# Optimization experiments

Hardware: AMD Instinct MI355X
Metric: run time of the kernel (lower is better)

## Reference

```python
import jax, jax.numpy as jnp
import numpy as np

B, NUM_OBJ, R, D, C = 1024, 128, 32, 512, 7  # scans, obj slots, rel samples, feat dim, rel classes
N = NUM_OBJ + R  # 160 graph nodes per scan


def setup_inputs() -> dict:
    key = jax.random.key(0)
    ks = jax.random.split(key, 8)
    obj_feats = jax.random.normal(ks[0], (B, NUM_OBJ, D), jnp.float32)
    pairs = jax.random.randint(ks[1], (B, R, 2), 0, NUM_OBJ, dtype=jnp.int32)
    init = lambda k, shape, fan_in: jax.random.normal(k, shape, jnp.float32) / np.float32(np.sqrt(fan_in))
    return {
        "obj_feats": obj_feats,
        "pairs": pairs,
        "fuse_w": init(ks[2], (2 * D, D), 2 * D), "fuse_b": jnp.zeros((D,), jnp.float32),
        "gcn_w": init(ks[3], (D, D), D), "gcn_b": jnp.zeros((D,), jnp.float32),
        "fc1_w": init(ks[4], (D, 256), D), "fc1_b": jnp.zeros((256,), jnp.float32),
        "fc2_w": init(ks[5], (256, 128), 256), "fc2_b": jnp.zeros((128,), jnp.float32),
        "fc3_w": init(ks[6], (128, C), 128), "fc3_b": jnp.zeros((C,), jnp.float32),
    }


def reference(obj_feats, pairs, fuse_w, fuse_b, gcn_w, gcn_b,
              fc1_w, fc1_b, fc2_w, fc2_b, fc3_w, fc3_b):
    # --- init_rel_node (pos_fuse=False): fuse sub/obj features per sampled pair ---
    sub = jnp.take_along_axis(obj_feats, pairs[:, :, 0:1], axis=1)  # [B,R,D]
    obj = jnp.take_along_axis(obj_feats, pairs[:, :, 1:2], axis=1)  # [B,R,D]
    init_rel = jnp.concatenate([sub, obj], axis=-1) @ fuse_w + fuse_b  # [B,R,D]

    # --- X: object node feats in rows [0,NUM_OBJ), rel node feats in rows [NUM_OBJ,N) ---
    X = jnp.concatenate([obj_feats, init_rel], axis=1)  # [B,N,D]

    # --- A: get_graph_gcn_with_rel -- scatter 4 directed edges per pair ---
    b_idx = jnp.arange(B)[:, None]                      # [B,1]
    ridx = NUM_OBJ + jnp.arange(R)[None, :]             # [1,R] rel node index j+num_obj
    p0, p1 = pairs[:, :, 0], pairs[:, :, 1]             # [B,R]
    A = jnp.zeros((B, N, N), jnp.float32)
    A = A.at[b_idx, p0, ridx].set(1.0)
    A = A.at[b_idx, ridx, p1].set(1.0)
    A = A.at[b_idx, p1, ridx].set(1.0)
    A = A.at[b_idx, ridx, p0].set(1.0)

    # --- simpleGCN: relu((A @ X) W + b) ---
    H = jax.nn.relu(jnp.einsum('bnm,bmd->bnd', A, X) @ gcn_w + gcn_b)  # [B,N,D]

    # --- residual: GCN rel-node output + init rel feats ---
    rel_feat = H[:, NUM_OBJ:, :] + init_rel  # [B,R,D]

    # --- proxi_detector (dropout = identity, eval behavior) ---
    h = jax.nn.relu(rel_feat @ fc1_w + fc1_b)
    h = jax.nn.relu(h @ fc2_w + fc2_b)
    logits = h @ fc3_w + fc3_b  # [B,R,C]
    return jax.nn.softmax(logits, axis=-1)
```

## Files before the change

kernel.cpp:

```cpp
#include <hip/hip_runtime.h>
#include <hip/hip_bf16.h>

#define B_    1024
#define NOBJ  128
#define RREL  32
#define DIM   512
#define MTOT  32768

typedef __bf16 bf16x8 __attribute__((ext_vector_type(8)));
typedef float  f32x4  __attribute__((ext_vector_type(4)));
typedef unsigned short us;

__device__ __forceinline__ us f2bf(float f) {
    unsigned int u = __float_as_uint(f);
    u += 0x7FFFu + ((u >> 16) & 1u);
    return (us)(u >> 16);
}
__device__ __forceinline__ float bf2f(us h) {
    return __uint_as_float(((unsigned int)h) << 16);
}

__device__ __forceinline__ void load16_to_lds(const us* g, us* l) {
    __builtin_amdgcn_global_load_lds((const __attribute__((address_space(1))) void*)g,
                                     (__attribute__((address_space(3))) void*)l,
                                     16, 0, 0);
}

__global__ __launch_bounds__(256) void gather_kernel(
        const float* __restrict__ obj, const int* __restrict__ pairs,
        us* __restrict__ As, us* __restrict__ Msum) {
    int t = threadIdx.x;
    int g = t >> 7;
    int c = t & 127;
    int base = blockIdx.x * 8;
#pragma unroll
    for (int rr = 0; rr < 4; ++rr) {
        int m  = base + rr * 2 + g;
        int b  = m >> 5;
        int p0 = pairs[(m << 1) + 0];
        int p1 = pairs[(m << 1) + 1];
        const float4* srow = (const float4*)(obj + (size_t)(b * NOBJ + p0) * DIM);
        const float4* orow = (const float4*)(obj + (size_t)(b * NOBJ + p1) * DIM);
        float4 s4 = srow[c];
        float4 o4 = orow[c];
        size_t arow = (size_t)m * 1024;
        ushort4 sb = make_ushort4(f2bf(s4.x), f2bf(s4.y), f2bf(s4.z), f2bf(s4.w));
        ushort4 ob = make_ushort4(f2bf(o4.x), f2bf(o4.y), f2bf(o4.z), f2bf(o4.w));
        *(ushort4*)(As + arow + c * 4)       = sb;
        *(ushort4*)(As + arow + 512 + c * 4) = ob;
        float4 mz = s4;
        if (p0 != p1) { mz.x += o4.x; mz.y += o4.y; mz.z += o4.z; mz.w += o4.w; }
        *(ushort4*)(Msum + (size_t)m * 512 + c * 4) =
            make_ushort4(f2bf(mz.x), f2bf(mz.y), f2bf(mz.z), f2bf(mz.w));
    }
}

__global__ __launch_bounds__(256) void prep_weights(
        const float* __restrict__ fw, const float* __restrict__ gw,
        const float* __restrict__ w1, const float* __restrict__ w2,
        us* __restrict__ WfT, us* __restrict__ WgT,
        us* __restrict__ W1T, us* __restrict__ W2T) {
    __shared__ float t32[32][33];
    int id = blockIdx.x;
    const float* in; us* out; int K, N, local;
    if (id < 512)      { in = fw; out = WfT; K = 1024; N = 512; local = id; }
    else if (id < 768) { in = gw; out = WgT; K = 512;  N = 512; local = id - 512; }
    else if (id < 896) { in = w1; out = W1T; K = 512;  N = 256; local = id - 768; }
    else               { in = w2; out = W2T; K = 256;  N = 128; local = id - 896; }
    int tilesN = N >> 5;
    int bk = (local / tilesN) * 32;
    int bn = (local % tilesN) * 32;
    int t  = threadIdx.x;
    int tx = t & 31, ty = t >> 5;
#pragma unroll
    for (int i = 0; i < 4; ++i)
        t32[ty + i * 8][tx] = in[(size_t)(bk + ty + i * 8) * N + bn + tx];
    __syncthreads();
#pragma unroll
    for (int i = 0; i < 4; ++i)
        out[(size_t)(bn + ty + i * 8) * K + bk + tx] = f2bf(t32[tx][ty + i * 8]);
}

__global__ __launch_bounds__(256, 2) void gemm_fused12(
        const us* __restrict__ As,
        const us* __restrict__ Msum,
        const us* __restrict__ WfT,
        const us* __restrict__ WgT,
        const float* __restrict__ fuse_b, const float* __restrict__ gcn_b,
        us* __restrict__ rf) {
    __shared__ __align__(16) us ldsA[128 * 32];
    __shared__ __align__(16) us ldsB[128 * 32];

    int tid  = threadIdx.x;
    int wid  = tid >> 6;
    int lane = tid & 63;
    int wm   = wid & 1;
    int wn   = wid >> 1;
    int m0   = blockIdx.x * 128;
    int n0   = blockIdx.y * 128;

    f32x4 accF[4][4], accG[4][4];
#pragma unroll
    for (int i = 0; i < 4; ++i)
#pragma unroll
        for (int j = 0; j < 4; ++j)
#pragma unroll
            for (int k = 0; k < 4; ++k) { accF[i][j][k] = 0.0f; accG[i][j][k] = 0.0f; }

    int r = tid >> 2, c = tid & 3;
    us* la0 = ldsA + wid * 512;
    us* la1 = ldsA + 2048 + wid * 512;
    us* lb0 = ldsB + wid * 512;
    us* lb1 = ldsB + 2048 + wid * 512;

    int arow = wm * 64 + (lane & 15);
    int brow = wn * 64 + (lane & 15);
    int koff = (lane >> 4) * 8;

    {
        const us* ag0 = As + (size_t)(m0 + r)      * 1024 + c * 8;
        const us* ag1 = As + (size_t)(m0 + 64 + r) * 1024 + c * 8;
        const us* bg0 = WfT + (size_t)(n0 + r)      * 1024 + c * 8;
        const us* bg1 = WfT + (size_t)(n0 + 64 + r) * 1024 + c * 8;
        for (int k0 = 0; k0 < 1024; k0 += 32) {
            __syncthreads();
            load16_to_lds(ag0 + k0, la0);
            load16_to_lds(ag1 + k0, la1);
            load16_to_lds(bg0 + k0, lb0);
            load16_to_lds(bg1 + k0, lb1);
            __syncthreads();
            bf16x8 a[4], b[4];
#pragma unroll
            for (int i = 0; i < 4; ++i)
                a[i] = *(const bf16x8*)(ldsA + (arow + i * 16) * 32 + koff);
#pragma unroll
            for (int j = 0; j < 4; ++j)
                b[j] = *(const bf16x8*)(ldsB + (brow + j * 16) * 32 + koff);
#pragma unroll
            for (int i = 0; i < 4; ++i)
#pragma unroll
                for (int j = 0; j < 4; ++j)
                    accF[i][j] = __builtin_amdgcn_mfma_f32_16x16x32_bf16(a[i], b[j], accF[i][j], 0, 0, 0);
        }
    }
    {
        const us* ag0 = Msum + (size_t)(m0 + r)      * 512 + c * 8;
        const us* ag1 = Msum + (size_t)(m0 + 64 + r) * 512 + c * 8;
        const us* bg0 = WgT + (size_t)(n0 + r)      * 512 + c * 8;
        const us* bg1 = WgT + (size_t)(n0 + 64 + r) * 512 + c * 8;
        for (int k0 = 0; k0 < 512; k0 += 32) {
            __syncthreads();
            load16_to_lds(ag0 + k0, la0);
            load16_to_lds(ag1 + k0, la1);
            load16_to_lds(bg0 + k0, lb0);
            load16_to_lds(bg1 + k0, lb1);
            __syncthreads();
            bf16x8 a[4], b[4];
#pragma unroll
            for (int i = 0; i < 4; ++i)
                a[i] = *(const bf16x8*)(ldsA + (arow + i * 16) * 32 + koff);
#pragma unroll
            for (int j = 0; j < 4; ++j)
                b[j] = *(const bf16x8*)(ldsB + (brow + j * 16) * 32 + koff);
#pragma unroll
            for (int i = 0; i < 4; ++i)
#pragma unroll
                for (int j = 0; j < 4; ++j)
                    accG[i][j] = __builtin_amdgcn_mfma_f32_16x16x32_bf16(a[i], b[j], accG[i][j], 0, 0, 0);
        }
    }

    int crow  = wm * 64 + (lane >> 4) * 4;
    int ccol0 = wn * 64 + (lane & 15);
    float bf_[4], bg_[4];
#pragma unroll
    for (int j = 0; j < 4; ++j) {
        bf_[j] = fuse_b[n0 + ccol0 + j * 16];
        bg_[j] = gcn_b [n0 + ccol0 + j * 16];
    }
#pragma unroll
    for (int i = 0; i < 4; ++i)
#pragma unroll
        for (int j = 0; j < 4; ++j) {
            int col = n0 + ccol0 + j * 16;
#pragma unroll
            for (int jj = 0; jj < 4; ++jj) {
                int row = m0 + crow + i * 16 + jj;
                float v = fmaxf(accG[i][j][jj] + bg_[j], 0.0f) + accF[i][j][jj] + bf_[j];
                rf[(size_t)row * 512 + col] = f2bf(v);
            }
        }
}

#define H1S 264
#define H2S 136
__global__ __launch_bounds__(256, 2) void tail_kernel(
        const us* __restrict__ rf,
        const us* __restrict__ W1T,
        const us* __restrict__ W2T,
        const float* __restrict__ b1, const float* __restrict__ b2,
        const float* __restrict__ w3, const float* __restrict__ b3,
        float* __restrict__ out) {
    __shared__ __align__(16) unsigned char pool[57888];
    us*    sA   = (us*)(pool);
    us*    sB   = (us*)(pool + 4096);
    us*    sH2  = (us*)(pool);
    us*    sH1  = (us*)(pool + 20480);
    float* sRed = (float*)(pool + 20480);
    float* sW3  = (float*)(pool + 54272);
    float* sB3  = (float*)(pool + 57856);

    int tid  = threadIdx.x;
    int wid  = tid >> 6;
    int lane = tid & 63;
    int m0   = blockIdx.x * 64;

    for (int i = tid; i < 128 * 7; i += 256) sW3[i] = w3[i];
    if (tid < 7) sB3[tid] = b3[tid];

    int r = tid >> 2, c = tid & 3;
    int koff = (lane >> 4) * 8;
    int l15  = lane & 15;

    f32x4 acc1[4][4];
#pragma unroll
    for (int i = 0; i < 4; ++i)
#pragma unroll
        for (int j = 0; j < 4; ++j)
#pragma unroll
            for (int k = 0; k < 4; ++k) acc1[i][j][k] = 0.0f;

    {
        const us* ag = rf + (size_t)(m0 + r) * 512 + c * 8;
        us* la = sA + wid * 512;
        for (int k0 = 0; k0 < 512; k0 += 32) {
            __syncthreads();
            load16_to_lds(ag + k0, la);
#pragma unroll
            for (int q = 0; q < 4; ++q)
                load16_to_lds(W1T + (size_t)(q * 64 + r) * 512 + k0 + c * 8,
                              sB + q * 2048 + wid * 512);
            __syncthreads();
            bf16x8 a[4], b[4];
#pragma unroll
            for (int i = 0; i < 4; ++i)
                a[i] = *(const bf16x8*)(sA + (l15 + i * 16) * 32 + koff);
#pragma unroll
            for (int j = 0; j < 4; ++j)
                b[j] = *(const bf16x8*)(sB + (wid * 64 + j * 16 + l15) * 32 + koff);
#pragma unroll
            for (int i = 0; i < 4; ++i)
#pragma unroll
                for (int j = 0; j < 4; ++j)
                    acc1[i][j] = __builtin_amdgcn_mfma_f32_16x16x32_bf16(a[i], b[j], acc1[i][j], 0, 0, 0);
        }
    }
#pragma unroll
    for (int i = 0; i < 4; ++i)
#pragma unroll
        for (int j = 0; j < 4; ++j) {
            int col = wid * 64 + j * 16 + l15;
            float bb = b1[col];
#pragma unroll
            for (int jj = 0; jj < 4; ++jj) {
                int row = i * 16 + (lane >> 4) * 4 + jj;
                sH1[row * H1S + col] = f2bf(fmaxf(acc1[i][j][jj] + bb, 0.0f));
            }
        }

    int nw = wid & 1, kw = wid >> 1;
    f32x4 acc2[4][4];
#pragma unroll
    for (int i = 0; i < 4; ++i)
#pragma unroll
        for (int j = 0; j < 4; ++j)
#pragma unroll
            for (int k = 0; k < 4; ++k) acc2[i][j][k] = 0.0f;

    for (int t = 0; t < 4; ++t) {
        __syncthreads();
#pragma unroll
        for (int s = 0; s < 2; ++s)
#pragma unroll
            for (int q = 0; q < 2; ++q)
                load16_to_lds(W2T + (size_t)(q * 64 + r) * 256 + s * 128 + t * 32 + c * 8,
                              sB + s * 4096 + q * 2048 + wid * 512);
        __syncthreads();
        bf16x8 a[4], b[4];
#pragma unroll
        for (int i = 0; i < 4; ++i)
            a[i] = *(const bf16x8*)(sH1 + (l15 + i * 16) * H1S + kw * 128 + t * 32 + koff);
#pragma unroll
        for (int j = 0; j < 4; ++j)
            b[j] = *(const bf16x8*)(sB + kw * 4096 + (nw * 64 + j * 16 + l15) * 32 + koff);
#pragma unroll
        for (int i = 0; i < 4; ++i)
#pragma unroll
            for (int j = 0; j < 4; ++j)
                acc2[i][j] = __builtin_amdgcn_mfma_f32_16x16x32_bf16(a[i], b[j], acc2[i][j], 0, 0, 0);
    }
    __syncthreads();
    if (kw == 1) {
#pragma unroll
        for (int i = 0; i < 4; ++i)
#pragma unroll
            for (int j = 0; j < 4; ++j) {
                int col = nw * 64 + j * 16 + l15;
#pragma unroll
                for (int jj = 0; jj < 4; ++jj) {
                    int row = i * 16 + (lane >> 4) * 4 + jj;
                    sRed[row * 132 + col] = acc2[i][j][jj];
                }
            }
    }
    __syncthreads();
    if (kw == 0) {
#pragma unroll
        for (int i = 0; i < 4; ++i)
#pragma unroll
            for (int j = 0; j < 4; ++j) {
                int col = nw * 64 + j * 16 + l15;
                float bb = b2[col];
#pragma unroll
                for (int jj = 0; jj < 4; ++jj) {
                    int row = i * 16 + (lane >> 4) * 4 + jj;
                    float v = acc2[i][j][jj] + sRed[row * 132 + col] + bb;
                    sH2[row * H2S + col] = f2bf(fmaxf(v, 0.0f));
                }
            }
    }
    __syncthreads();

    int row = tid >> 2;
    int p   = tid & 3;
    float accv[7];
#pragma unroll
    for (int cc = 0; cc < 7; ++cc) accv[cc] = 0.0f;
    const us* hrow = sH2 + row * H2S + p * 32;
    for (int kk = 0; kk < 8; ++kk) {
        ushort4 u = *(const ushort4*)(hrow + kk * 4);
        float f0 = bf2f(u.x), f1 = bf2f(u.y), f2 = bf2f(u.z), f3 = bf2f(u.w);
        int k = p * 32 + kk * 4;
#pragma unroll
        for (int cc = 0; cc < 7; ++cc) {
            accv[cc] = fmaf(f0, sW3[(k + 0) * 7 + cc], accv[cc]);
            accv[cc] = fmaf(f1, sW3[(k + 1) * 7 + cc], accv[cc]);
            accv[cc] = fmaf(f2, sW3[(k + 2) * 7 + cc], accv[cc]);
            accv[cc] = fmaf(f3, sW3[(k + 3) * 7 + cc], accv[cc]);
        }
    }
#pragma unroll
    for (int cc = 0; cc < 7; ++cc) {
        accv[cc] += __shfl_xor(accv[cc], 1);
        accv[cc] += __shfl_xor(accv[cc], 2);
    }
    if (p == 0) {
        float mx = accv[0] + sB3[0];
        float lg[7];
#pragma unroll
        for (int cc = 0; cc < 7; ++cc) { lg[cc] = accv[cc] + sB3[cc]; mx = fmaxf(mx, lg[cc]); }
        float sum = 0.f;
#pragma unroll
        for (int cc = 0; cc < 7; ++cc) { lg[cc] = __expf(lg[cc] - mx); sum += lg[cc]; }
        float inv = 1.0f / sum;
#pragma unroll
        for (int cc = 0; cc < 7; ++cc) out[(size_t)(m0 + row) * 7 + cc] = lg[cc] * inv;
    }
}

extern "C" void kernel_launch(void* const* d_in, const int* in_sizes, int n_in,
                              void* d_out, int out_size, void* d_ws, size_t ws_size,
                              hipStream_t stream) {
    (void)in_sizes; (void)n_in; (void)out_size; (void)ws_size;
    const float* obj    = (const float*)d_in[0];
    const int*   pairs  = (const int*)  d_in[1];
    const float* fuse_w = (const float*)d_in[2];
    const float* fuse_b = (const float*)d_in[3];
    const float* gcn_w  = (const float*)d_in[4];
    const float* gcn_b  = (const float*)d_in[5];
    const float* fc1_w  = (const float*)d_in[6];
    const float* fc1_b  = (const float*)d_in[7];
    const float* fc2_w  = (const float*)d_in[8];
    const float* fc2_b  = (const float*)d_in[9];
    const float* fc3_w  = (const float*)d_in[10];
    const float* fc3_b  = (const float*)d_in[11];
    float* out = (float*)d_out;

    char* ws = (char*)d_ws;
    us* As   = (us*)(ws);
    us* Msum = (us*)(ws + (64u  << 20));
    us* rf   = (us*)(ws + (96u  << 20));
    us* WfT  = (us*)(ws + (128u << 20));
    us* WgT  = (us*)(ws + (129u << 20));
    us* W1T  = (us*)(ws + (130u << 20));
    us* W2T  = (us*)(ws + (131u << 20));

    gather_kernel<<<MTOT / 8, 256, 0, stream>>>(obj, pairs, As, Msum);
    prep_weights<<<928, 256, 0, stream>>>(fuse_w, gcn_w, fc1_w, fc2_w,
                                          WfT, WgT, W1T, W2T);

    gemm_fused12<<<dim3(MTOT / 128, 4), 256, 0, stream>>>(
        As, Msum, WfT, WgT, fuse_b, gcn_b, rf);

    tail_kernel<<<MTOT / 64, 256, 0, stream>>>(
        rf, W1T, W2T, fc1_b, fc2_b, fc3_w, fc3_b, out);
}
```

Before: 447.7 us.

## Fuse pair gather and bf16 conversion into the GEMM A-tile loads

Removes the separate gather kernel and its bf16 As/Msum intermediates. The GEMM now reads fp32 object rows directly through the pair indices, converts them to bf16 in registers, and builds the summed GCN input on the fly before storing to LDS. The grid is also transposed so the four N-tiles that share an M-tile run next to each other and can reuse the gathered fp32 rows in L2. In exchange, each block re-reads fp32 data at twice the bytes of bf16, and the loads are now plain register loads followed by a conversion instead of direct global-to-LDS copies.

```diff
diff --git a/kernel.cpp b/kernel.cpp
--- a/kernel.cpp
+++ b/kernel.cpp
@@ -26,33 +26,11 @@
                                      16, 0, 0);
 }
 
-__global__ __launch_bounds__(256) void gather_kernel(
-        const float* __restrict__ obj, const int* __restrict__ pairs,
-        us* __restrict__ As, us* __restrict__ Msum) {
-    int t = threadIdx.x;
-    int g = t >> 7;
-    int c = t & 127;
-    int base = blockIdx.x * 8;
-#pragma unroll
-    for (int rr = 0; rr < 4; ++rr) {
-        int m  = base + rr * 2 + g;
-        int b  = m >> 5;
-        int p0 = pairs[(m << 1) + 0];
-        int p1 = pairs[(m << 1) + 1];
-        const float4* srow = (const float4*)(obj + (size_t)(b * NOBJ + p0) * DIM);
-        const float4* orow = (const float4*)(obj + (size_t)(b * NOBJ + p1) * DIM);
-        float4 s4 = srow[c];
-        float4 o4 = orow[c];
-        size_t arow = (size_t)m * 1024;
-        ushort4 sb = make_ushort4(f2bf(s4.x), f2bf(s4.y), f2bf(s4.z), f2bf(s4.w));
-        ushort4 ob = make_ushort4(f2bf(o4.x), f2bf(o4.y), f2bf(o4.z), f2bf(o4.w));
-        *(ushort4*)(As + arow + c * 4)       = sb;
-        *(ushort4*)(As + arow + 512 + c * 4) = ob;
-        float4 mz = s4;
-        if (p0 != p1) { mz.x += o4.x; mz.y += o4.y; mz.z += o4.z; mz.w += o4.w; }
-        *(ushort4*)(Msum + (size_t)m * 512 + c * 4) =
-            make_ushort4(f2bf(mz.x), f2bf(mz.y), f2bf(mz.z), f2bf(mz.w));
-    }
+__device__ __forceinline__ bf16x8 cvt8(float4 a, float4 b) {
+    bf16x8 v;
+    v[0] = (__bf16)a.x; v[1] = (__bf16)a.y; v[2] = (__bf16)a.z; v[3] = (__bf16)a.w;
+    v[4] = (__bf16)b.x; v[5] = (__bf16)b.y; v[6] = (__bf16)b.z; v[7] = (__bf16)b.w;
+    return v;
 }
 
 __global__ __launch_bounds__(256) void prep_weights(
@@ -82,8 +60,8 @@
 }
 
 __global__ __launch_bounds__(256, 2) void gemm_fused12(
-        const us* __restrict__ As,
-        const us* __restrict__ Msum,
+        const float* __restrict__ obj,
+        const int*   __restrict__ pairs,
         const us* __restrict__ WfT,
         const us* __restrict__ WgT,
         const float* __restrict__ fuse_b, const float* __restrict__ gcn_b,
@@ -96,8 +74,8 @@
     int lane = tid & 63;
     int wm   = wid & 1;
     int wn   = wid >> 1;
-    int m0   = blockIdx.x * 128;
-    int n0   = blockIdx.y * 128;
+    int n0   = blockIdx.x * 128;
+    int m0   = blockIdx.y * 128;
 
     f32x4 accF[4][4], accG[4][4];
 #pragma unroll
@@ -108,8 +86,19 @@
             for (int k = 0; k < 4; ++k) { accF[i][j][k] = 0.0f; accG[i][j][k] = 0.0f; }
 
     int r = tid >> 2, c = tid & 3;
-    us* la0 = ldsA + wid * 512;
-    us* la1 = ldsA + 2048 + wid * 512;
+
+    int ma = m0 + r, mb = m0 + 64 + r;
+    int2 pa = ((const int2*)pairs)[ma];
+    int2 pb = ((const int2*)pairs)[mb];
+    const float* sA_ = obj + ((size_t)((ma >> 5) * NOBJ) + pa.x) * DIM;
+    const float* oA_ = obj + ((size_t)((ma >> 5) * NOBJ) + pa.y) * DIM;
+    const float* sB_ = obj + ((size_t)((mb >> 5) * NOBJ) + pb.x) * DIM;
+    const float* oB_ = obj + ((size_t)((mb >> 5) * NOBJ) + pb.y) * DIM;
+    float flA = (pa.x != pa.y) ? 1.0f : 0.0f;
+    float flB = (pb.x != pb.y) ? 1.0f : 0.0f;
+
+    us* la0 = ldsA + tid * 8;
+    us* la1 = ldsA + 2048 + tid * 8;
     us* lb0 = ldsB + wid * 512;
     us* lb1 = ldsB + 2048 + wid * 512;
 
@@ -118,14 +107,19 @@
     int koff = (lane >> 4) * 8;
 
     {
-        const us* ag0 = As + (size_t)(m0 + r)      * 1024 + c * 8;
-        const us* ag1 = As + (size_t)(m0 + 64 + r) * 1024 + c * 8;
         const us* bg0 = WfT + (size_t)(n0 + r)      * 1024 + c * 8;
         const us* bg1 = WfT + (size_t)(n0 + 64 + r) * 1024 + c * 8;
         for (int k0 = 0; k0 < 1024; k0 += 32) {
-            __syncthreads();
-            load16_to_lds(ag0 + k0, la0);
-            load16_to_lds(ag1 + k0, la1);
+            int kk = k0 & 511;
+            const float* p0 = (k0 < 512) ? sA_ : oA_;
+            const float* p1 = (k0 < 512) ? sB_ : oB_;
+            float4 x0 = *(const float4*)(p0 + kk + c * 8);
+            float4 x1 = *(const float4*)(p0 + kk + c * 8 + 4);
+            float4 y0 = *(const float4*)(p1 + kk + c * 8);
+            float4 y1 = *(const float4*)(p1 + kk + c * 8 + 4);
+            __syncthreads();
+            *(bf16x8*)la0 = cvt8(x0, x1);
+            *(bf16x8*)la1 = cvt8(y0, y1);
             load16_to_lds(bg0 + k0, lb0);
             load16_to_lds(bg1 + k0, lb1);
             __syncthreads();
@@ -144,14 +138,33 @@
         }
     }
     {
-        const us* ag0 = Msum + (size_t)(m0 + r)      * 512 + c * 8;
-        const us* ag1 = Msum + (size_t)(m0 + 64 + r) * 512 + c * 8;
         const us* bg0 = WgT + (size_t)(n0 + r)      * 512 + c * 8;
         const us* bg1 = WgT + (size_t)(n0 + 64 + r) * 512 + c * 8;
         for (int k0 = 0; k0 < 512; k0 += 32) {
-            __syncthreads();
-            load16_to_lds(ag0 + k0, la0);
-            load16_to_lds(ag1 + k0, la1);
+            const float* a0 = sA_ + k0 + c * 8;
+            const float* a1 = oA_ + k0 + c * 8;
+            const float* b0 = sB_ + k0 + c * 8;
+            const float* b1 = oB_ + k0 + c * 8;
+            float4 sx = *(const float4*)(a0);
+            float4 sy = *(const float4*)(a0 + 4);
+            float4 ox = *(const float4*)(a1);
+            float4 oy = *(const float4*)(a1 + 4);
+            float4 tx = *(const float4*)(b0);
+            float4 ty = *(const float4*)(b0 + 4);
+            float4 ux = *(const float4*)(b1);
+            float4 uy = *(const float4*)(b1 + 4);
+            __syncthreads();
+            float4 m0v, m1v, m2v, m3v;
+            m0v.x = fmaf(flA, ox.x, sx.x); m0v.y = fmaf(flA, ox.y, sx.y);
+            m0v.z = fmaf(flA, ox.z, sx.z); m0v.w = fmaf(flA, ox.w, sx.w);
+            m1v.x = fmaf(flA, oy.x, sy.x); m1v.y = fmaf(flA, oy.y, sy.y);
+            m1v.z = fmaf(flA, oy.z, sy.z); m1v.w = fmaf(flA, oy.w, sy.w);
+            m2v.x = fmaf(flB, ux.x, tx.x); m2v.y = fmaf(flB, ux.y, tx.y);
+            m2v.z = fmaf(flB, ux.z, tx.z); m2v.w = fmaf(flB, ux.w, tx.w);
+            m3v.x = fmaf(flB, uy.x, ty.x); m3v.y = fmaf(flB, uy.y, ty.y);
+            m3v.z = fmaf(flB, uy.z, ty.z); m3v.w = fmaf(flB, uy.w, ty.w);
+            *(bf16x8*)la0 = cvt8(m0v, m1v);
+            *(bf16x8*)la1 = cvt8(m2v, m3v);
             load16_to_lds(bg0 + k0, lb0);
             load16_to_lds(bg1 + k0, lb1);
             __syncthreads();
@@ -387,20 +400,17 @@
     float* out = (float*)d_out;
 
     char* ws = (char*)d_ws;
-    us* As   = (us*)(ws);
-    us* Msum = (us*)(ws + (64u  << 20));
-    us* rf   = (us*)(ws + (96u  << 20));
-    us* WfT  = (us*)(ws + (128u << 20));
-    us* WgT  = (us*)(ws + (129u << 20));
-    us* W1T  = (us*)(ws + (130u << 20));
-    us* W2T  = (us*)(ws + (131u << 20));
-
-    gather_kernel<<<MTOT / 8, 256, 0, stream>>>(obj, pairs, As, Msum);
+    us* rf   = (us*)(ws);
+    us* WfT  = (us*)(ws + (32u << 20));
+    us* WgT  = (us*)(ws + (34u << 20));
+    us* W1T  = (us*)(ws + (35u << 20));
+    us* W2T  = (us*)(ws + (36u << 20));
+
     prep_weights<<<928, 256, 0, stream>>>(fuse_w, gcn_w, fc1_w, fc2_w,
                                           WfT, WgT, W1T, W2T);
 
-    gemm_fused12<<<dim3(MTOT / 128, 4), 256, 0, stream>>>(
-        As, Msum, WfT, WgT, fuse_b, gcn_b, rf);
+    gemm_fused12<<<dim3(4, MTOT / 128), 256, 0, stream>>>(
+        obj, pairs, WfT, WgT, fuse_b, gcn_b, rf);
 
     tail_kernel<<<MTOT / 64, 256, 0, stream>>>(
         rf, W1T, W2T, fc1_b, fc2_b, fc3_w, fc3_b, out);
```

Result: slower. 479.7 us (+7.1%).

## Merge fused GEMM k-loops into one 48KB-stage loop and swap grid order

Applied to the files above, without the earlier changes.

The two sequential k-loops (1024-deep fuse GEMM and 512-deep GCN GEMM) become a single 16-iteration loop. Each iteration stages six 128x32 tiles (both halves of A and WfT, plus Msum and WgT) into a 48KB LDS buffer and runs three MFMA groups per barrier pair. This cuts the number of barriers by a factor of three and gives more loads in flight per stage. The grid is also transposed so that the four N-blocks sharing an M tile launch next to each other, which should improve L2 reuse of the A rows. The larger LDS footprint may reduce occupancy from the requested 2 blocks per CU.

```diff
diff --git a/kernel.cpp b/kernel.cpp
--- a/kernel.cpp
+++ b/kernel.cpp
@@ -88,16 +88,15 @@
         const us* __restrict__ WgT,
         const float* __restrict__ fuse_b, const float* __restrict__ gcn_b,
         us* __restrict__ rf) {
-    __shared__ __align__(16) us ldsA[128 * 32];
-    __shared__ __align__(16) us ldsB[128 * 32];
+    __shared__ __align__(16) us lds[6 * 4096];
 
     int tid  = threadIdx.x;
     int wid  = tid >> 6;
     int lane = tid & 63;
     int wm   = wid & 1;
     int wn   = wid >> 1;
-    int m0   = blockIdx.x * 128;
-    int n0   = blockIdx.y * 128;
+    int n0   = blockIdx.x * 128;
+    int m0   = blockIdx.y * 128;
 
     f32x4 accF[4][4], accG[4][4];
 #pragma unroll
@@ -108,65 +107,65 @@
             for (int k = 0; k < 4; ++k) { accF[i][j][k] = 0.0f; accG[i][j][k] = 0.0f; }
 
     int r = tid >> 2, c = tid & 3;
-    us* la0 = ldsA + wid * 512;
-    us* la1 = ldsA + 2048 + wid * 512;
-    us* lb0 = ldsB + wid * 512;
-    us* lb1 = ldsB + 2048 + wid * 512;
+    const us* alo0 = As   + (size_t)(m0 + r)      * 1024 + c * 8;
+    const us* alo1 = As   + (size_t)(m0 + 64 + r) * 1024 + c * 8;
+    const us* ahi0 = alo0 + 512;
+    const us* ahi1 = alo1 + 512;
+    const us* ms0  = Msum + (size_t)(m0 + r)      * 512 + c * 8;
+    const us* ms1  = Msum + (size_t)(m0 + 64 + r) * 512 + c * 8;
+    const us* flo0 = WfT  + (size_t)(n0 + r)      * 1024 + c * 8;
+    const us* flo1 = WfT  + (size_t)(n0 + 64 + r) * 1024 + c * 8;
+    const us* fhi0 = flo0 + 512;
+    const us* fhi1 = flo1 + 512;
+    const us* gg0  = WgT  + (size_t)(n0 + r)      * 512 + c * 8;
+    const us* gg1  = WgT  + (size_t)(n0 + 64 + r) * 512 + c * 8;
+
+    us* wb = lds + wid * 512;
 
     int arow = wm * 64 + (lane & 15);
     int brow = wn * 64 + (lane & 15);
     int koff = (lane >> 4) * 8;
 
-    {
-        const us* ag0 = As + (size_t)(m0 + r)      * 1024 + c * 8;
-        const us* ag1 = As + (size_t)(m0 + 64 + r) * 1024 + c * 8;
-        const us* bg0 = WfT + (size_t)(n0 + r)      * 1024 + c * 8;
-        const us* bg1 = WfT + (size_t)(n0 + 64 + r) * 1024 + c * 8;
-        for (int k0 = 0; k0 < 1024; k0 += 32) {
-            __syncthreads();
-            load16_to_lds(ag0 + k0, la0);
-            load16_to_lds(ag1 + k0, la1);
-            load16_to_lds(bg0 + k0, lb0);
-            load16_to_lds(bg1 + k0, lb1);
-            __syncthreads();
+    for (int k0 = 0; k0 < 512; k0 += 32) {
+        __syncthreads();
+        load16_to_lds(alo0 + k0, wb);
+        load16_to_lds(alo1 + k0, wb + 2048);
+        load16_to_lds(ahi0 + k0, wb + 4096);
+        load16_to_lds(ahi1 + k0, wb + 6144);
+        load16_to_lds(ms0  + k0, wb + 8192);
+        load16_to_lds(ms1  + k0, wb + 10240);
+        load16_to_lds(flo0 + k0, wb + 12288);
+        load16_to_lds(flo1 + k0, wb + 14336);
+        load16_to_lds(fhi0 + k0, wb + 16384);
+        load16_to_lds(fhi1 + k0, wb + 18432);
+        load16_to_lds(gg0  + k0, wb + 20480);
+        load16_to_lds(gg1  + k0, wb + 22528);
+        __syncthreads();
+
+#pragma unroll
+        for (int t = 0; t < 3; ++t) {
+            const us* tA = lds + t * 4096;
+            const us* tB = lds + 12288 + t * 4096;
             bf16x8 a[4], b[4];
 #pragma unroll
             for (int i = 0; i < 4; ++i)
-                a[i] = *(const bf16x8*)(ldsA + (arow + i * 16) * 32 + koff);
+                a[i] = *(const bf16x8*)(tA + (arow + i * 16) * 32 + koff);
 #pragma unroll
             for (int j = 0; j < 4; ++j)
-                b[j] = *(const bf16x8*)(ldsB + (brow + j * 16) * 32 + koff);
-#pragma unroll
-            for (int i = 0; i < 4; ++i)
-#pragma unroll
-                for (int j = 0; j < 4; ++j)
-                    accF[i][j] = __builtin_amdgcn_mfma_f32_16x16x32_bf16(a[i], b[j], accF[i][j], 0, 0, 0);
-        }
-    }
-    {
-        const us* ag0 = Msum + (size_t)(m0 + r)      * 512 + c * 8;
-        const us* ag1 = Msum + (size_t)(m0 + 64 + r) * 512 + c * 8;
-        const us* bg0 = WgT + (size_t)(n0 + r)      * 512 + c * 8;
-        const us* bg1 = WgT + (size_t)(n0 + 64 + r) * 512 + c * 8;
-        for (int k0 = 0; k0 < 512; k0 += 32) {
-            __syncthreads();
-            load16_to_lds(ag0 + k0, la0);
-            load16_to_lds(ag1 + k0, la1);
-            load16_to_lds(bg0 + k0, lb0);
-            load16_to_lds(bg1 + k0, lb1);
-            __syncthreads();
-            bf16x8 a[4], b[4];
-#pragma unroll
-            for (int i = 0; i < 4; ++i)
-                a[i] = *(const bf16x8*)(ldsA + (arow + i * 16) * 32 + koff);
-#pragma unroll
-            for (int j = 0; j < 4; ++j)
-                b[j] = *(const bf16x8*)(ldsB + (brow + j * 16) * 32 + koff);
-#pragma unroll
-            for (int i = 0; i < 4; ++i)
-#pragma unroll
-                for (int j = 0; j < 4; ++j)
-                    accG[i][j] = __builtin_amdgcn_mfma_f32_16x16x32_bf16(a[i], b[j], accG[i][j], 0, 0, 0);
+                b[j] = *(const bf16x8*)(tB + (brow + j * 16) * 32 + koff);
+            if (t < 2) {
+#pragma unroll
+                for (int i = 0; i < 4; ++i)
+#pragma unroll
+                    for (int j = 0; j < 4; ++j)
+                        accF[i][j] = __builtin_amdgcn_mfma_f32_16x16x32_bf16(a[i], b[j], accF[i][j], 0, 0, 0);
+            } else {
+#pragma unroll
+                for (int i = 0; i < 4; ++i)
+#pragma unroll
+                    for (int j = 0; j < 4; ++j)
+                        accG[i][j] = __builtin_amdgcn_mfma_f32_16x16x32_bf16(a[i], b[j], accG[i][j], 0, 0, 0);
+            }
         }
     }
 
@@ -399,7 +398,7 @@
     prep_weights<<<928, 256, 0, stream>>>(fuse_w, gcn_w, fc1_w, fc2_w,
                                           WfT, WgT, W1T, W2T);
 
-    gemm_fused12<<<dim3(MTOT / 128, 4), 256, 0, stream>>>(
+    gemm_fused12<<<dim3(4, MTOT / 128), 256, 0, stream>>>(
         As, Msum, WfT, WgT, fuse_b, gcn_b, rf);
 
     tail_kernel<<<MTOT / 64, 256, 0, stream>>>(
```

New measurement: 456.1 us. No clear change (+1.9%).
